# Kernel tuning notes

Hardware: AMD Instinct MI355X
Metric: run time of the kernel (lower is better)

Reference implementation:

```python
import jax, jax.numpy as jnp
import numpy as np

jax.config.update("jax_enable_x64", True)  # original casts to double for cov/cholesky

B, C, H, W, DR = 64, 2048, 14, 14, 256
EPS = 1e-6      # LCMCOV eps added to covariance diagonal
BN_EPS = 1e-5   # torch BatchNorm2d default eps


def setup_inputs() -> dict:
    key = jax.random.key(0)
    k0, k1 = jax.random.split(key)
    x = jax.random.normal(k0, (B, C, H, W), dtype=jnp.float32)
    # 1x1 conv weight (kaiming fan_out for relu): std = sqrt(2 / fan_out), fan_out = DR*1*1... torch uses fan_out = out_ch*k*k per output; approximate with sqrt(2/C) scale on (DR, C)
    w_conv = jax.random.normal(k1, (DR, C), dtype=jnp.float32) * np.sqrt(2.0 / C).astype(np.float32)
    gamma = jnp.ones((DR,), jnp.float32)
    beta = jnp.zeros((DR,), jnp.float32)
    run_mean = jnp.zeros((DR,), jnp.float32)
    run_var = jnp.ones((DR,), jnp.float32)
    return {"x": x, "w_conv": w_conv, "gamma": gamma, "beta": beta,
            "run_mean": run_mean, "run_var": run_var}


def reference(x, w_conv, gamma, beta, run_mean, run_var):
    b, c, h, w = x.shape
    dr = w_conv.shape[0]
    m = h * w
    # 1x1 conv (no bias) + BatchNorm2d (eval mode, running stats) + ReLU
    y = jnp.einsum('bchw,dc->bdhw', x, w_conv)
    scale = gamma / jnp.sqrt(run_var + BN_EPS)
    y = y * scale[None, :, None, None] + (beta - run_mean * scale)[None, :, None, None]
    y = jax.nn.relu(y)
    # Covpool in float64: x I_hat x^T == (1/M) * (x - mean)(x - mean)^T
    xd = y.reshape(b, dr, m).astype(jnp.float64)
    xc = xd - xd.mean(axis=2, keepdims=True)  # [B, DR, M]
    cov = jnp.einsum('bdm,bem->bde', xc, xc) / m  # [B, DR, DR]
    # LogI_LCM: Cholesky, log the diagonal, symmetrize
    cov = cov + EPS * jnp.eye(dr, dtype=jnp.float64)
    L = jnp.linalg.cholesky(cov)
    diag = jnp.log(jnp.diagonal(L, axis1=-2, axis2=-1))          # [B, DR]
    tril = jnp.tril(L, -1) + jnp.eye(dr, dtype=L.dtype) * diag[:, :, None]
    sym = tril + jnp.swapaxes(tril, -1, -2)
    # Triuvec: upper-triangular (incl diag) entries in row-major order, cast to float32
    iu, ju = jnp.triu_indices(dr)
    return sym[:, iu, ju].astype(jnp.float32)  # [B, DR*(DR+1)/2]
```

## Files before the change

kernel.cpp:

```cpp
#include <hip/hip_runtime.h>
#include <math.h>

#define BB 64
#define CC 2048
#define MM 196
#define DD 256
#define NTOT (BB * MM)

typedef __attribute__((ext_vector_type(8))) short short8;
typedef __attribute__((ext_vector_type(4))) short short4v;
typedef __attribute__((ext_vector_type(4))) unsigned short ushort4v;
typedef __attribute__((ext_vector_type(4))) float f32x4;

__device__ __forceinline__ unsigned short bf16_rne(float f) {
  unsigned int u = __float_as_uint(f);
  unsigned int r = u + 0x7FFFu + ((u >> 16) & 1u);
  return (unsigned short)(r >> 16);
}

__global__ __launch_bounds__(256) void k_prep(
    const float* __restrict__ w, const float* __restrict__ gamma,
    const float* __restrict__ beta, const float* __restrict__ rmean,
    const float* __restrict__ rvar, unsigned short* __restrict__ wh,
    unsigned short* __restrict__ wl, float* __restrict__ sclv,
    float* __restrict__ sftv) {
  const int e0 = (blockIdx.x * 256 + threadIdx.x) * 4;
  f32x4 v = *(const f32x4*)(w + e0);
  ushort4v h, l;
#pragma unroll
  for (int i = 0; i < 4; ++i) {
    unsigned short hb = bf16_rne(v[i]);
    float hf = __uint_as_float((unsigned int)hb << 16);
    h[i] = hb;
    l[i] = bf16_rne(v[i] - hf);
  }
  *(ushort4v*)(wh + e0) = h;
  *(ushort4v*)(wl + e0) = l;
  if (blockIdx.x == 0 && threadIdx.x < DD) {
    int d = threadIdx.x;
    float s = gamma[d] / sqrtf(rvar[d] + 1e-5f);
    sclv[d] = s;
    sftv[d] = beta[d] - rmean[d] * s;
  }
}

__global__ __launch_bounds__(256, 2) void k_conv(
    const float* __restrict__ x, const unsigned short* __restrict__ wh,
    const unsigned short* __restrict__ wl, const float* __restrict__ sclv,
    const float* __restrict__ sftv, float* __restrict__ yt) {
  const int tid = threadIdx.x;
  const int wid = tid >> 6, lane = tid & 63;
  const int quad = lane >> 4, l16 = lane & 15;
  const int n0 = blockIdx.x * 64;

  __shared__ unsigned short Xh[64][36];
  __shared__ unsigned short Xl[64][36];

  f32x4 acc[4][4];
#pragma unroll
  for (int i = 0; i < 4; ++i)
#pragma unroll
    for (int j = 0; j < 4; ++j) acc[i][j] = (f32x4)0.f;

  const int nX = tid & 63, kq = tid >> 6;
  const int gn = n0 + nX;
  const int bX = gn / MM, mX = gn - bX * MM;
  const float* xp = x + (size_t)bX * CC * MM + mX;

  float xr[8];
#pragma unroll
  for (int p = 0; p < 8; ++p) xr[p] = xp[(size_t)(kq * 8 + p) * MM];

  size_t aoff[4];
#pragma unroll
  for (int ds = 0; ds < 4; ++ds)
    aoff[ds] = (size_t)(wid * 64 + ds * 16 + l16) * CC + quad * 8;

  short8 Ah[4], Al[4], Ah2[4], Al2[4];
#pragma unroll
  for (int ds = 0; ds < 4; ++ds) {
    Ah[ds] = *(const short8*)(wh + aoff[ds]);
    Al[ds] = *(const short8*)(wl + aoff[ds]);
  }

  for (int c = 0; c < 64; ++c) {
    const int k0 = c * 32;
    __syncthreads();
    {
      ushort4v h0, h1, l0, l1;
#pragma unroll
      for (int p = 0; p < 4; ++p) {
        unsigned short hb = bf16_rne(xr[p]);
        float hf = __uint_as_float((unsigned int)hb << 16);
        h0[p] = hb;
        l0[p] = bf16_rne(xr[p] - hf);
      }
#pragma unroll
      for (int p = 0; p < 4; ++p) {
        unsigned short hb = bf16_rne(xr[4 + p]);
        float hf = __uint_as_float((unsigned int)hb << 16);
        h1[p] = hb;
        l1[p] = bf16_rne(xr[4 + p] - hf);
      }
      *(ushort4v*)&Xh[nX][kq * 8] = h0;
      *(ushort4v*)&Xh[nX][kq * 8 + 4] = h1;
      *(ushort4v*)&Xl[nX][kq * 8] = l0;
      *(ushort4v*)&Xl[nX][kq * 8 + 4] = l1;
    }
    __syncthreads();
    if (c < 63) {
#pragma unroll
      for (int p = 0; p < 8; ++p)
        xr[p] = xp[(size_t)(k0 + 32 + kq * 8 + p) * MM];
#pragma unroll
      for (int ds = 0; ds < 4; ++ds) {
        Ah2[ds] = *(const short8*)(wh + aoff[ds] + k0 + 32);
        Al2[ds] = *(const short8*)(wl + aoff[ds] + k0 + 32);
      }
    }
#pragma unroll
    for (int ns = 0; ns < 4; ++ns) {
      const unsigned short* bp = &Xh[ns * 16 + l16][quad * 8];
      short4v b0 = *(const short4v*)bp;
      short4v b1 = *(const short4v*)(bp + 4);
      short8 Bh = __builtin_shufflevector(b0, b1, 0, 1, 2, 3, 4, 5, 6, 7);
      const unsigned short* bq = &Xl[ns * 16 + l16][quad * 8];
      short4v c0 = *(const short4v*)bq;
      short4v c1 = *(const short4v*)(bq + 4);
      short8 Bl = __builtin_shufflevector(c0, c1, 0, 1, 2, 3, 4, 5, 6, 7);
#pragma unroll
      for (int ds = 0; ds < 4; ++ds) {
        acc[ds][ns] = __builtin_amdgcn_mfma_f32_16x16x32_bf16(
            Ah[ds], Bh, acc[ds][ns], 0, 0, 0);
        acc[ds][ns] = __builtin_amdgcn_mfma_f32_16x16x32_bf16(
            Ah[ds], Bl, acc[ds][ns], 0, 0, 0);
        acc[ds][ns] = __builtin_amdgcn_mfma_f32_16x16x32_bf16(
            Al[ds], Bh, acc[ds][ns], 0, 0, 0);
      }
    }
#pragma unroll
    for (int ds = 0; ds < 4; ++ds) {
      Ah[ds] = Ah2[ds];
      Al[ds] = Al2[ds];
    }
  }

#pragma unroll
  for (int ds = 0; ds < 4; ++ds) {
    const int dbase = wid * 64 + ds * 16 + quad * 4;
    f32x4 s4 = *(const f32x4*)(sclv + dbase);
    f32x4 f4 = *(const f32x4*)(sftv + dbase);
#pragma unroll
    for (int ns = 0; ns < 4; ++ns) {
      const int n = n0 + ns * 16 + l16;
      const int b = n / MM, m = n - b * MM;
      f32x4 o;
#pragma unroll
      for (int r = 0; r < 4; ++r) {
        float v = fmaf(acc[ds][ns][r], s4[r], f4[r]);
        o[r] = v > 0.f ? v : 0.f;
      }
      *(f32x4*)(yt + ((size_t)b * MM + m) * DD + dbase) = o;
    }
  }
}

__global__ __launch_bounds__(256) void k_means(const float* __restrict__ yt,
                                               double* __restrict__ mean) {
  const int b = blockIdx.x;
  const int d = threadIdx.x;
  const float* p = yt + (size_t)b * MM * DD + d;
  double s0 = 0, s1 = 0, s2 = 0, s3 = 0;
  for (int m = 0; m < MM; m += 4) {
    s0 += (double)p[(size_t)(m + 0) * DD];
    s1 += (double)p[(size_t)(m + 1) * DD];
    s2 += (double)p[(size_t)(m + 2) * DD];
    s3 += (double)p[(size_t)(m + 3) * DD];
  }
  mean[b * DD + d] = (s0 + s1 + s2 + s3) * (1.0 / MM);
}

__global__ __launch_bounds__(256) void k_cov(const float* __restrict__ yt,
                                             const double* __restrict__ mean,
                                             double* __restrict__ cov) {
  const int b = blockIdx.x;
  const int t = blockIdx.y;
  const int ti = (t < 1) ? 0 : (t < 3) ? 1 : (t < 6) ? 2 : 3;
  const int tj = t - (ti * (ti + 1)) / 2;
  const int i0 = ti * 64, j0 = tj * 64;
  const int tid = threadIdx.x;
  const int tx = tid & 15, ty = tid >> 4;

  __shared__ double As[32][66];
  __shared__ double Bs[32][66];

  double acc[4][4];
#pragma unroll
  for (int i = 0; i < 4; ++i)
#pragma unroll
    for (int j = 0; j < 4; ++j) acc[i][j] = 0.0;

  const int dl = tid & 63, kl = tid >> 6;
  const double mA = mean[b * DD + i0 + dl];
  const double mB = mean[b * DD + j0 + dl];
  const float* ybase = yt + (size_t)b * MM * DD;

  for (int k0 = 0; k0 < MM; k0 += 32) {
    __syncthreads();
#pragma unroll
    for (int p = 0; p < 8; ++p) {
      int k = kl + p * 4;
      int m = k0 + k;
      double av = 0.0, bv = 0.0;
      if (m < MM) {
        av = (double)ybase[(size_t)m * DD + i0 + dl] - mA;
        bv = (double)ybase[(size_t)m * DD + j0 + dl] - mB;
      }
      As[k][dl] = av;
      Bs[k][dl] = bv;
    }
    __syncthreads();
#pragma unroll
    for (int k = 0; k < 32; ++k) {
      double a[4], bv[4];
#pragma unroll
      for (int i = 0; i < 4; ++i) a[i] = As[k][ty * 4 + i];
#pragma unroll
      for (int j = 0; j < 4; ++j) bv[j] = Bs[k][tx * 4 + j];
#pragma unroll
      for (int i = 0; i < 4; ++i)
#pragma unroll
        for (int j = 0; j < 4; ++j) acc[i][j] = fma(a[i], bv[j], acc[i][j]);
    }
  }

  double* cb = cov + (size_t)b * DD * DD;
#pragma unroll
  for (int i = 0; i < 4; ++i) {
#pragma unroll
    for (int j = 0; j < 4; ++j) {
      int gi = i0 + ty * 4 + i, gj = j0 + tx * 4 + j;
      double v = acc[i][j] * (1.0 / MM);
      if (gi == gj) v += 1e-6;
      cb[(size_t)gi * DD + gj] = v;
      if (ti != tj) cb[(size_t)gj * DD + gi] = v;
    }
  }
}

__global__ __launch_bounds__(256) void k_panel3(double* __restrict__ cov,
                                                float* __restrict__ out,
                                                int kb) {
  const int b = blockIdx.x;
  double* A = cov + (size_t)b * DD * DD;
  const int j0 = kb * 32;
  const int tid = threadIdx.x;

  __shared__ double sh[4224];

  if (blockIdx.y == 0) {
    double(*LpTop)[33] = (double(*)[33])sh;
    double(*L11s)[33] = (double(*)[33])(sh + 1056);
    double* rpivs = sh + 2112;
    const int R = DD - j0;
    const int pj = j0 - 32;

    double sp[32];
    const double* rowp = A + (size_t)(j0 + tid) * DD;
    if (tid < R) {
#pragma unroll
      for (int c = 0; c < 32; ++c) sp[c] = rowp[j0 + c];
    }

    if (kb > 0) {
      double lp[32];
      if (tid < R) {
#pragma unroll
        for (int c = 0; c < 32; ++c) lp[c] = rowp[pj + c];
      }
      if (tid < 32) {
#pragma unroll
        for (int c = 0; c < 32; ++c) LpTop[tid][c] = lp[c];
      }
      __syncthreads();
      if (tid < R) {
#pragma unroll
        for (int c = 0; c < 32; ++c) {
          double a = 0.0;
#pragma unroll
          for (int p = 0; p < 32; ++p) a = fma(lp[p], LpTop[c][p], a);
          sp[c] -= a;
        }
      }
    }

    if (tid < 32) {
      double rpkeep = 0.0;
#pragma unroll
      for (int j = 0; j < 32; ++j) {
        double dj = __shfl(sp[j], j);
        double piv = sqrt(dj);
        double rp = 1.0 / piv;
        if (tid == j) {
          sp[j] = piv;
          rpkeep = rp;
        } else {
          sp[j] = sp[j] * rp;
        }
        double lij = sp[j];
#pragma unroll
        for (int k = j + 1; k < 32; ++k) {
          double ck = __shfl(lij, k);
          sp[k] -= lij * ck;
        }
      }
#pragma unroll
      for (int k = 0; k < 32; ++k) L11s[tid][k] = (k <= tid) ? sp[k] : 0.0;
      rpivs[tid] = rpkeep;
      for (int k = 0; k <= tid; ++k)
        A[(size_t)(j0 + tid) * DD + j0 + k] = sp[k];
    }
    __syncthreads();

    if (tid >= 32 && tid < R) {
#pragma unroll
      for (int j = 0; j < 32; ++j) {
        double s = sp[j];
#pragma unroll
        for (int k = 0; k < 32; ++k)
          if (k < j) s -= sp[k] * L11s[j][k];
        sp[j] = s * rpivs[j];
      }
      double* dst = A + (size_t)(j0 + tid) * DD + j0;
#pragma unroll
      for (int k = 0; k < 32; ++k) dst[k] = sp[k];
    }

    if (kb == 7) {
      float* Sf = (float*)sh;
      __syncthreads();
      for (int t = 0; t < 10; ++t) {
        int ti = 0, tj = t;
        while (tj >= 4 - ti) {
          tj -= (4 - ti);
          ti++;
        }
        tj += ti;
        __syncthreads();
        for (int e = tid; e < 4096; e += 256) {
          int jj = e >> 6, ii = e & 63;
          Sf[jj * 65 + ii] =
              (float)A[(size_t)(tj * 64 + jj) * DD + ti * 64 + ii];
        }
        __syncthreads();
        for (int e = tid; e < 4096; e += 256) {
          int ii = e >> 6, jj = e & 63;
          int i = ti * 64 + ii, j = tj * 64 + jj;
          if (j < i) continue;
          float v = Sf[jj * 65 + ii];
          if (i == j) v = 2.0f * logf(v);
          int off = i * DD - (i * (i - 1)) / 2 + (j - i);
          out[(size_t)b * 32896 + off] = v;
        }
      }
    }
  } else {
    const int o = j0 + 32;
    const int S = DD - o;
    const int pj = j0 - 32;
    int tI = 0, tJ = (int)blockIdx.y - 1;
    while (tJ > tI) {
      tJ -= (tI + 1);
      tI++;
    }
    const int i0 = tI * 64, jj0 = tJ * 64;
    const int txl = tid & 15, tyl = tid >> 4;

    double(*Ea)[33] = (double(*)[33])sh;
    double(*Eb)[33] = (double(*)[33])(sh + 2112);

    for (int e = tid; e < 64 * 32; e += 256) {
      int r = e >> 5, c = e & 31;
      Ea[r][c] = (i0 + r < S) ? A[(size_t)(o + i0 + r) * DD + pj + c] : 0.0;
      Eb[r][c] = (jj0 + r < S) ? A[(size_t)(o + jj0 + r) * DD + pj + c] : 0.0;
    }
    __syncthreads();

    double s[4][4];
#pragma unroll
    for (int i = 0; i < 4; ++i)
#pragma unroll
      for (int j = 0; j < 4; ++j) s[i][j] = 0.0;

    const int bi = tyl * 4, bj = txl * 4;
#pragma unroll
    for (int k = 0; k < 32; ++k) {
      double a[4], bv[4];
#pragma unroll
      for (int i = 0; i < 4; ++i) a[i] = Ea[bi + i][k];
#pragma unroll
      for (int j = 0; j < 4; ++j) bv[j] = Eb[bj + j][k];
#pragma unroll
      for (int i = 0; i < 4; ++i)
#pragma unroll
        for (int j = 0; j < 4; ++j) s[i][j] = fma(a[i], bv[j], s[i][j]);
    }

#pragma unroll
    for (int i = 0; i < 4; ++i)
#pragma unroll
      for (int j = 0; j < 4; ++j) {
        int gi = i0 + bi + i, gj = jj0 + bj + j;
        if (gi < S && gj < S && gi >= gj)
          A[(size_t)(o + gi) * DD + (o + gj)] -= s[i][j];
      }
  }
}

extern "C" void kernel_launch(void* const* d_in, const int* in_sizes, int n_in,
                              void* d_out, int out_size, void* d_ws,
                              size_t ws_size, hipStream_t stream) {
  const float* x = (const float*)d_in[0];
  const float* w = (const float*)d_in[1];
  const float* gamma = (const float*)d_in[2];
  const float* beta = (const float*)d_in[3];
  const float* rmean = (const float*)d_in[4];
  const float* rvar = (const float*)d_in[5];
  float* out = (float*)d_out;

  char* ws = (char*)d_ws;
  float* yt = (float*)ws;
  double* mean = (double*)(ws + 12845056);
  double* cov = (double*)(ws + 12845056 + 131072);
  unsigned short* wh = (unsigned short*)cov;
  unsigned short* wl = wh + (DD * CC);
  float* sclv = (float*)(wl + (DD * CC));
  float* sftv = sclv + DD;

  k_prep<<<512, 256, 0, stream>>>(w, gamma, beta, rmean, rvar, wh, wl, sclv,
                                  sftv);
  k_conv<<<NTOT / 64, 256, 0, stream>>>(x, wh, wl, sclv, sftv, yt);
  k_means<<<BB, 256, 0, stream>>>(yt, mean);
  k_cov<<<dim3(BB, 10), 256, 0, stream>>>(yt, mean, cov);
  for (int kb = 0; kb < 8; ++kb) {
    int ntiles = 0;
    if (kb > 0) {
      int S = DD - (kb * 32 + 32);
      if (S > 0) {
        int nt = (S + 63) / 64;
        ntiles = nt * (nt + 1) / 2;
      }
    }
    k_panel3<<<dim3(BB, 1 + ntiles), 256, 0, stream>>>(cov, out, kb);
  }
}
```

Baseline: 639.2 us.

## Replace eight per-panel Cholesky launches with one persistent kernel using atomic flags

The blocked Cholesky used to run as eight separate kernel launches, one per 32-column panel. These are merged into a single persistent kernel. Within each batch, panel and trailing-update blocks coordinate through global atomic counters stored in the first words of that batch's output buffer. The counters are zeroed in k_means. This removes launch gaps and lets panel work overlap with updates. In exchange it relies on spin-waiting, which can deadlock if the blocks are not co-resident, and it temporarily uses output memory as flags until the final write-out overwrites them.

```diff
diff --git a/kernel.cpp b/kernel.cpp
--- a/kernel.cpp
+++ b/kernel.cpp
@@ -166,9 +166,11 @@
 }
 
 __global__ __launch_bounds__(256) void k_means(const float* __restrict__ yt,
-                                               double* __restrict__ mean) {
+                                               double* __restrict__ mean,
+                                               float* __restrict__ out) {
   const int b = blockIdx.x;
   const int d = threadIdx.x;
+  if (d < 16) ((int*)(out + (size_t)b * 32896))[d] = 0;
   const float* p = yt + (size_t)b * MM * DD + d;
   double s0 = 0, s1 = 0, s2 = 0, s3 = 0;
   for (int m = 0; m < MM; m += 4) {
@@ -248,13 +250,37 @@
   }
 }
 
-__global__ __launch_bounds__(256) void k_panel3(double* __restrict__ cov,
-                                                float* __restrict__ out,
-                                                int kb) {
+__device__ __forceinline__ void block_wait(int* p, int target) {
+  if (threadIdx.x == 0) {
+    while (__hip_atomic_load(p, __ATOMIC_RELAXED, __HIP_MEMORY_SCOPE_AGENT) <
+           target)
+      __builtin_amdgcn_s_sleep(1);
+  }
+  __syncthreads();
+  __builtin_amdgcn_fence(__ATOMIC_ACQUIRE, "agent");
+}
+
+__device__ __forceinline__ void block_signal(int* p) {
+  __syncthreads();
+  if (threadIdx.x == 0)
+    __hip_atomic_fetch_add(p, 1, __ATOMIC_RELEASE, __HIP_MEMORY_SCOPE_AGENT);
+}
+
+__device__ __forceinline__ int ntiles_of(int s) {
+  int S = 224 - 32 * s;
+  if (S <= 0) return 0;
+  int nt = (S + 63) >> 6;
+  return nt * (nt + 1) / 2;
+}
+
+__global__ __launch_bounds__(256, 2) void k_persist(double* __restrict__ cov,
+                                                    float* out) {
   const int b = blockIdx.x;
+  const int tid = threadIdx.x;
   double* A = cov + (size_t)b * DD * DD;
-  const int j0 = kb * 32;
-  const int tid = threadIdx.x;
+  int* flg = (int*)(out + (size_t)b * 32896);
+  int* P = flg;
+  int* T = flg + 8;
 
   __shared__ double sh[4224];
 
@@ -262,158 +288,173 @@
     double(*LpTop)[33] = (double(*)[33])sh;
     double(*L11s)[33] = (double(*)[33])(sh + 1056);
     double* rpivs = sh + 2112;
-    const int R = DD - j0;
-    const int pj = j0 - 32;
-
-    double sp[32];
-    const double* rowp = A + (size_t)(j0 + tid) * DD;
-    if (tid < R) {
-#pragma unroll
-      for (int c = 0; c < 32; ++c) sp[c] = rowp[j0 + c];
-    }
-
-    if (kb > 0) {
-      double lp[32];
+
+    for (int kb = 0; kb < 8; ++kb) {
+      const int j0 = kb * 32;
+      const int R = DD - j0;
+      const int pj = j0 - 32;
+      if (kb >= 2) block_wait(&T[kb - 1], ntiles_of(kb - 1));
+
+      double sp[32];
+      const double* rowp = A + (size_t)(j0 + tid) * DD;
       if (tid < R) {
 #pragma unroll
-        for (int c = 0; c < 32; ++c) lp[c] = rowp[pj + c];
-      }
+        for (int c = 0; c < 32; ++c) sp[c] = rowp[j0 + c];
+      }
+
+      if (kb > 0) {
+        double lp[32];
+        if (tid < R) {
+#pragma unroll
+          for (int c = 0; c < 32; ++c) lp[c] = rowp[pj + c];
+        }
+        __syncthreads();
+        if (tid < 32) {
+#pragma unroll
+          for (int c = 0; c < 32; ++c) LpTop[tid][c] = lp[c];
+        }
+        __syncthreads();
+        if (tid < R) {
+#pragma unroll
+          for (int c = 0; c < 32; ++c) {
+            double a = 0.0;
+#pragma unroll
+            for (int p = 0; p < 32; ++p) a = fma(lp[p], LpTop[c][p], a);
+            sp[c] -= a;
+          }
+        }
+      }
+
       if (tid < 32) {
-#pragma unroll
-        for (int c = 0; c < 32; ++c) LpTop[tid][c] = lp[c];
+        double rpkeep = 0.0;
+#pragma unroll
+        for (int j = 0; j < 32; ++j) {
+          double dj = __shfl(sp[j], j);
+          double piv = sqrt(dj);
+          double rp = 1.0 / piv;
+          if (tid == j) {
+            sp[j] = piv;
+            rpkeep = rp;
+          } else {
+            sp[j] = sp[j] * rp;
+          }
+          double lij = sp[j];
+#pragma unroll
+          for (int k = j + 1; k < 32; ++k) {
+            double ck = __shfl(lij, k);
+            sp[k] -= lij * ck;
+          }
+        }
+#pragma unroll
+        for (int k = 0; k < 32; ++k) L11s[tid][k] = (k <= tid) ? sp[k] : 0.0;
+        rpivs[tid] = rpkeep;
+        for (int k = 0; k <= tid; ++k)
+          A[(size_t)(j0 + tid) * DD + j0 + k] = sp[k];
       }
       __syncthreads();
-      if (tid < R) {
-#pragma unroll
-        for (int c = 0; c < 32; ++c) {
-          double a = 0.0;
-#pragma unroll
-          for (int p = 0; p < 32; ++p) a = fma(lp[p], LpTop[c][p], a);
-          sp[c] -= a;
-        }
-      }
-    }
-
-    if (tid < 32) {
-      double rpkeep = 0.0;
-#pragma unroll
-      for (int j = 0; j < 32; ++j) {
-        double dj = __shfl(sp[j], j);
-        double piv = sqrt(dj);
-        double rp = 1.0 / piv;
-        if (tid == j) {
-          sp[j] = piv;
-          rpkeep = rp;
-        } else {
-          sp[j] = sp[j] * rp;
-        }
-        double lij = sp[j];
-#pragma unroll
-        for (int k = j + 1; k < 32; ++k) {
-          double ck = __shfl(lij, k);
-          sp[k] -= lij * ck;
-        }
-      }
-#pragma unroll
-      for (int k = 0; k < 32; ++k) L11s[tid][k] = (k <= tid) ? sp[k] : 0.0;
-      rpivs[tid] = rpkeep;
-      for (int k = 0; k <= tid; ++k)
-        A[(size_t)(j0 + tid) * DD + j0 + k] = sp[k];
-    }
-    __syncthreads();
-
-    if (tid >= 32 && tid < R) {
-#pragma unroll
-      for (int j = 0; j < 32; ++j) {
-        double s = sp[j];
-#pragma unroll
-        for (int k = 0; k < 32; ++k)
-          if (k < j) s -= sp[k] * L11s[j][k];
-        sp[j] = s * rpivs[j];
-      }
-      double* dst = A + (size_t)(j0 + tid) * DD + j0;
-#pragma unroll
-      for (int k = 0; k < 32; ++k) dst[k] = sp[k];
-    }
-
-    if (kb == 7) {
-      float* Sf = (float*)sh;
+
+      if (tid >= 32 && tid < R) {
+#pragma unroll
+        for (int j = 0; j < 32; ++j) {
+          double s = sp[j];
+#pragma unroll
+          for (int k = 0; k < 32; ++k)
+            if (k < j) s -= sp[k] * L11s[j][k];
+          sp[j] = s * rpivs[j];
+        }
+        double* dst = A + (size_t)(j0 + tid) * DD + j0;
+#pragma unroll
+        for (int k = 0; k < 32; ++k) dst[k] = sp[k];
+      }
+      block_signal(&P[kb]);
+    }
+
+    float* Sf = (float*)sh;
+    for (int t = 0; t < 10; ++t) {
+      int ti = 0, tj = t;
+      while (tj >= 4 - ti) {
+        tj -= (4 - ti);
+        ti++;
+      }
+      tj += ti;
       __syncthreads();
-      for (int t = 0; t < 10; ++t) {
-        int ti = 0, tj = t;
-        while (tj >= 4 - ti) {
-          tj -= (4 - ti);
-          ti++;
-        }
-        tj += ti;
-        __syncthreads();
-        for (int e = tid; e < 4096; e += 256) {
-          int jj = e >> 6, ii = e & 63;
-          Sf[jj * 65 + ii] =
-              (float)A[(size_t)(tj * 64 + jj) * DD + ti * 64 + ii];
-        }
-        __syncthreads();
-        for (int e = tid; e < 4096; e += 256) {
-          int ii = e >> 6, jj = e & 63;
-          int i = ti * 64 + ii, j = tj * 64 + jj;
-          if (j < i) continue;
-          float v = Sf[jj * 65 + ii];
-          if (i == j) v = 2.0f * logf(v);
-          int off = i * DD - (i * (i - 1)) / 2 + (j - i);
-          out[(size_t)b * 32896 + off] = v;
-        }
+      for (int e = tid; e < 4096; e += 256) {
+        int jj = e >> 6, ii = e & 63;
+        Sf[jj * 65 + ii] =
+            (float)A[(size_t)(tj * 64 + jj) * DD + ti * 64 + ii];
+      }
+      __syncthreads();
+      for (int e = tid; e < 4096; e += 256) {
+        int ii = e >> 6, jj = e & 63;
+        int i = ti * 64 + ii, j = tj * 64 + jj;
+        if (j < i) continue;
+        float v = Sf[jj * 65 + ii];
+        if (i == j) v = 2.0f * logf(v);
+        int off = i * DD - (i * (i - 1)) / 2 + (j - i);
+        out[(size_t)b * 32896 + off] = v;
       }
     }
   } else {
-    const int o = j0 + 32;
-    const int S = DD - o;
-    const int pj = j0 - 32;
-    int tI = 0, tJ = (int)blockIdx.y - 1;
-    while (tJ > tI) {
-      tJ -= (tI + 1);
-      tI++;
-    }
-    const int i0 = tI * 64, jj0 = tJ * 64;
-    const int txl = tid & 15, tyl = tid >> 4;
-
+    const int w = (int)blockIdx.y - 1;
     double(*Ea)[33] = (double(*)[33])sh;
     double(*Eb)[33] = (double(*)[33])(sh + 2112);
-
-    for (int e = tid; e < 64 * 32; e += 256) {
-      int r = e >> 5, c = e & 31;
-      Ea[r][c] = (i0 + r < S) ? A[(size_t)(o + i0 + r) * DD + pj + c] : 0.0;
-      Eb[r][c] = (jj0 + r < S) ? A[(size_t)(o + jj0 + r) * DD + pj + c] : 0.0;
-    }
-    __syncthreads();
-
-    double s[4][4];
-#pragma unroll
-    for (int i = 0; i < 4; ++i)
-#pragma unroll
-      for (int j = 0; j < 4; ++j) s[i][j] = 0.0;
-
+    const int txl = tid & 15, tyl = tid >> 4;
     const int bi = tyl * 4, bj = txl * 4;
-#pragma unroll
-    for (int k = 0; k < 32; ++k) {
-      double a[4], bv[4];
-#pragma unroll
-      for (int i = 0; i < 4; ++i) a[i] = Ea[bi + i][k];
-#pragma unroll
-      for (int j = 0; j < 4; ++j) bv[j] = Eb[bj + j][k];
+
+    for (int s = 1; s <= 6; ++s) {
+      if (w >= ntiles_of(s)) continue;
+      block_wait(&P[s - 1], 1);
+      if (s >= 2) block_wait(&T[s - 1], ntiles_of(s - 1));
+
+      const int j0 = s * 32;
+      const int o = j0 + 32;
+      const int S = DD - o;
+      const int pj = j0 - 32;
+      int tI = 0, tJ = w;
+      while (tJ > tI) {
+        tJ -= (tI + 1);
+        tI++;
+      }
+      const int i0 = tI * 64, jj0 = tJ * 64;
+
+      for (int e = tid; e < 64 * 32; e += 256) {
+        int r = e >> 5, c = e & 31;
+        Ea[r][c] = (i0 + r < S) ? A[(size_t)(o + i0 + r) * DD + pj + c] : 0.0;
+        Eb[r][c] =
+            (jj0 + r < S) ? A[(size_t)(o + jj0 + r) * DD + pj + c] : 0.0;
+      }
+      __syncthreads();
+
+      double sacc[4][4];
 #pragma unroll
       for (int i = 0; i < 4; ++i)
 #pragma unroll
-        for (int j = 0; j < 4; ++j) s[i][j] = fma(a[i], bv[j], s[i][j]);
-    }
-
-#pragma unroll
-    for (int i = 0; i < 4; ++i)
-#pragma unroll
-      for (int j = 0; j < 4; ++j) {
-        int gi = i0 + bi + i, gj = jj0 + bj + j;
-        if (gi < S && gj < S && gi >= gj)
-          A[(size_t)(o + gi) * DD + (o + gj)] -= s[i][j];
-      }
+        for (int j = 0; j < 4; ++j) sacc[i][j] = 0.0;
+
+#pragma unroll
+      for (int k = 0; k < 32; ++k) {
+        double a[4], bv[4];
+#pragma unroll
+        for (int i = 0; i < 4; ++i) a[i] = Ea[bi + i][k];
+#pragma unroll
+        for (int j = 0; j < 4; ++j) bv[j] = Eb[bj + j][k];
+#pragma unroll
+        for (int i = 0; i < 4; ++i)
+#pragma unroll
+          for (int j = 0; j < 4; ++j)
+            sacc[i][j] = fma(a[i], bv[j], sacc[i][j]);
+      }
+
+#pragma unroll
+      for (int i = 0; i < 4; ++i)
+#pragma unroll
+        for (int j = 0; j < 4; ++j) {
+          int gi = i0 + bi + i, gj = jj0 + bj + j;
+          if (gi < S && gj < S && gi >= gj)
+            A[(size_t)(o + gi) * DD + (o + gj)] -= sacc[i][j];
+        }
+      block_signal(&T[s]);
+    }
   }
 }
 
@@ -440,17 +481,7 @@
   k_prep<<<512, 256, 0, stream>>>(w, gamma, beta, rmean, rvar, wh, wl, sclv,
                                   sftv);
   k_conv<<<NTOT / 64, 256, 0, stream>>>(x, wh, wl, sclv, sftv, yt);
-  k_means<<<BB, 256, 0, stream>>>(yt, mean);
+  k_means<<<BB, 256, 0, stream>>>(yt, mean, out);
   k_cov<<<dim3(BB, 10), 256, 0, stream>>>(yt, mean, cov);
-  for (int kb = 0; kb < 8; ++kb) {
-    int ntiles = 0;
-    if (kb > 0) {
-      int S = DD - (kb * 32 + 32);
-      if (S > 0) {
-        int nt = (S + 63) / 64;
-        ntiles = nt * (nt + 1) / 2;
-      }
-    }
-    k_panel3<<<dim3(BB, 1 + ntiles), 256, 0, stream>>>(cov, out, kb);
-  }
-}
+  k_persist<<<dim3(BB, 7), 256, 0, stream>>>(cov, out);
+}
```

New measurement: 998.9 us. 56.3% more time.

## Double-buffer conv LDS tiles and fold mean computation into covariance kernel

Applied to the files above, without the earlier changes.

The conv kernel now keeps two LDS buffers for the split bf16 X tile, so the next tile is written while MFMAs read the current one, leaving one barrier per iteration instead of two. The separate means kernel is removed and each covariance block computes the means it needs for its row and column slices directly from yt into shared memory. This saves a kernel launch and overlaps staging with compute. In exchange it doubles conv LDS use, and the ten tile blocks per batch each recompute the same means, adding redundant reads of yt.

```diff
diff --git a/kernel.cpp b/kernel.cpp
--- a/kernel.cpp
+++ b/kernel.cpp
@@ -53,8 +53,8 @@
   const int quad = lane >> 4, l16 = lane & 15;
   const int n0 = blockIdx.x * 64;
 
-  __shared__ unsigned short Xh[64][36];
-  __shared__ unsigned short Xl[64][36];
+  __shared__ unsigned short Xh[2][64][36];
+  __shared__ unsigned short Xl[2][64][36];
 
   f32x4 acc[4][4];
 #pragma unroll
@@ -67,10 +67,6 @@
   const int bX = gn / MM, mX = gn - bX * MM;
   const float* xp = x + (size_t)bX * CC * MM + mX;
 
-  float xr[8];
-#pragma unroll
-  for (int p = 0; p < 8; ++p) xr[p] = xp[(size_t)(kq * 8 + p) * MM];
-
   size_t aoff[4];
 #pragma unroll
   for (int ds = 0; ds < 4; ++ds)
@@ -83,10 +79,37 @@
     Al[ds] = *(const short8*)(wl + aoff[ds]);
   }
 
+  float xr[8];
+#pragma unroll
+  for (int p = 0; p < 8; ++p) xr[p] = xp[(size_t)(kq * 8 + p) * MM];
+  {
+    ushort4v h0, h1, l0, l1;
+#pragma unroll
+    for (int p = 0; p < 4; ++p) {
+      unsigned short hb = bf16_rne(xr[p]);
+      float hf = __uint_as_float((unsigned int)hb << 16);
+      h0[p] = hb;
+      l0[p] = bf16_rne(xr[p] - hf);
+    }
+#pragma unroll
+    for (int p = 0; p < 4; ++p) {
+      unsigned short hb = bf16_rne(xr[4 + p]);
+      float hf = __uint_as_float((unsigned int)hb << 16);
+      h1[p] = hb;
+      l1[p] = bf16_rne(xr[4 + p] - hf);
+    }
+    *(ushort4v*)&Xh[0][nX][kq * 8] = h0;
+    *(ushort4v*)&Xh[0][nX][kq * 8 + 4] = h1;
+    *(ushort4v*)&Xl[0][nX][kq * 8] = l0;
+    *(ushort4v*)&Xl[0][nX][kq * 8 + 4] = l1;
+  }
+#pragma unroll
+  for (int p = 0; p < 8; ++p) xr[p] = xp[(size_t)(32 + kq * 8 + p) * MM];
+  __syncthreads();
+
   for (int c = 0; c < 64; ++c) {
-    const int k0 = c * 32;
-    __syncthreads();
-    {
+    const int buf = c & 1;
+    if (c < 63) {
       ushort4v h0, h1, l0, l1;
 #pragma unroll
       for (int p = 0; p < 4; ++p) {
@@ -102,29 +125,28 @@
         h1[p] = hb;
         l1[p] = bf16_rne(xr[4 + p] - hf);
       }
-      *(ushort4v*)&Xh[nX][kq * 8] = h0;
-      *(ushort4v*)&Xh[nX][kq * 8 + 4] = h1;
-      *(ushort4v*)&Xl[nX][kq * 8] = l0;
-      *(ushort4v*)&Xl[nX][kq * 8 + 4] = l1;
-    }
-    __syncthreads();
-    if (c < 63) {
-#pragma unroll
-      for (int p = 0; p < 8; ++p)
-        xr[p] = xp[(size_t)(k0 + 32 + kq * 8 + p) * MM];
+      *(ushort4v*)&Xh[buf ^ 1][nX][kq * 8] = h0;
+      *(ushort4v*)&Xh[buf ^ 1][nX][kq * 8 + 4] = h1;
+      *(ushort4v*)&Xl[buf ^ 1][nX][kq * 8] = l0;
+      *(ushort4v*)&Xl[buf ^ 1][nX][kq * 8 + 4] = l1;
+      if (c < 62) {
+#pragma unroll
+        for (int p = 0; p < 8; ++p)
+          xr[p] = xp[(size_t)((c + 2) * 32 + kq * 8 + p) * MM];
+      }
 #pragma unroll
       for (int ds = 0; ds < 4; ++ds) {
-        Ah2[ds] = *(const short8*)(wh + aoff[ds] + k0 + 32);
-        Al2[ds] = *(const short8*)(wl + aoff[ds] + k0 + 32);
+        Ah2[ds] = *(const short8*)(wh + aoff[ds] + (c + 1) * 32);
+        Al2[ds] = *(const short8*)(wl + aoff[ds] + (c + 1) * 32);
       }
     }
 #pragma unroll
     for (int ns = 0; ns < 4; ++ns) {
-      const unsigned short* bp = &Xh[ns * 16 + l16][quad * 8];
+      const unsigned short* bp = &Xh[buf][ns * 16 + l16][quad * 8];
       short4v b0 = *(const short4v*)bp;
       short4v b1 = *(const short4v*)(bp + 4);
       short8 Bh = __builtin_shufflevector(b0, b1, 0, 1, 2, 3, 4, 5, 6, 7);
-      const unsigned short* bq = &Xl[ns * 16 + l16][quad * 8];
+      const unsigned short* bq = &Xl[buf][ns * 16 + l16][quad * 8];
       short4v c0 = *(const short4v*)bq;
       short4v c1 = *(const short4v*)(bq + 4);
       short8 Bl = __builtin_shufflevector(c0, c1, 0, 1, 2, 3, 4, 5, 6, 7);
@@ -138,10 +160,13 @@
             Al[ds], Bh, acc[ds][ns], 0, 0, 0);
       }
     }
-#pragma unroll
-    for (int ds = 0; ds < 4; ++ds) {
-      Ah[ds] = Ah2[ds];
-      Al[ds] = Al2[ds];
+    __syncthreads();
+    if (c < 63) {
+#pragma unroll
+      for (int ds = 0; ds < 4; ++ds) {
+        Ah[ds] = Ah2[ds];
+        Al[ds] = Al2[ds];
+      }
     }
   }
 
@@ -165,23 +190,7 @@
   }
 }
 
-__global__ __launch_bounds__(256) void k_means(const float* __restrict__ yt,
-                                               double* __restrict__ mean) {
-  const int b = blockIdx.x;
-  const int d = threadIdx.x;
-  const float* p = yt + (size_t)b * MM * DD + d;
-  double s0 = 0, s1 = 0, s2 = 0, s3 = 0;
-  for (int m = 0; m < MM; m += 4) {
-    s0 += (double)p[(size_t)(m + 0) * DD];
-    s1 += (double)p[(size_t)(m + 1) * DD];
-    s2 += (double)p[(size_t)(m + 2) * DD];
-    s3 += (double)p[(size_t)(m + 3) * DD];
-  }
-  mean[b * DD + d] = (s0 + s1 + s2 + s3) * (1.0 / MM);
-}
-
 __global__ __launch_bounds__(256) void k_cov(const float* __restrict__ yt,
-                                             const double* __restrict__ mean,
                                              double* __restrict__ cov) {
   const int b = blockIdx.x;
   const int t = blockIdx.y;
@@ -193,6 +202,7 @@
 
   __shared__ double As[32][66];
   __shared__ double Bs[32][66];
+  __shared__ double Ms[4][64];
 
   double acc[4][4];
 #pragma unroll
@@ -201,9 +211,20 @@
     for (int j = 0; j < 4; ++j) acc[i][j] = 0.0;
 
   const int dl = tid & 63, kl = tid >> 6;
-  const double mA = mean[b * DD + i0 + dl];
-  const double mB = mean[b * DD + j0 + dl];
   const float* ybase = yt + (size_t)b * MM * DD;
+
+  {
+    const int base_d = ((kl < 2) ? i0 : j0) + dl;
+    const int mlo = (kl & 1) ? 98 : 0;
+    const int mhi = (kl & 1) ? 196 : 98;
+    double s = 0.0;
+    for (int m = mlo; m < mhi; ++m)
+      s += (double)ybase[(size_t)m * DD + base_d];
+    Ms[kl][dl] = s;
+  }
+  __syncthreads();
+  const double mA = (Ms[0][dl] + Ms[1][dl]) * (1.0 / MM);
+  const double mB = (Ms[2][dl] + Ms[3][dl]) * (1.0 / MM);
 
   for (int k0 = 0; k0 < MM; k0 += 32) {
     __syncthreads();
@@ -430,7 +451,6 @@
 
   char* ws = (char*)d_ws;
   float* yt = (float*)ws;
-  double* mean = (double*)(ws + 12845056);
   double* cov = (double*)(ws + 12845056 + 131072);
   unsigned short* wh = (unsigned short*)cov;
   unsigned short* wl = wh + (DD * CC);
@@ -440,8 +460,7 @@
   k_prep<<<512, 256, 0, stream>>>(w, gamma, beta, rmean, rvar, wh, wl, sclv,
                                   sftv);
   k_conv<<<NTOT / 64, 256, 0, stream>>>(x, wh, wl, sclv, sftv, yt);
-  k_means<<<BB, 256, 0, stream>>>(yt, mean);
-  k_cov<<<dim3(BB, 10), 256, 0, stream>>>(yt, mean, cov);
+  k_cov<<<dim3(BB, 10), 256, 0, stream>>>(yt, cov);
   for (int kb = 0; kb < 8; ++kb) {
     int ntiles = 0;
     if (kb > 0) {
```

After: 652.5 us. +2.1%, slower.
